# Performance work log

Hardware: AMD Instinct MI355X
Metric: run time of the kernel (lower is better)

The kernel has to match this reference:

```python
import jax, jax.numpy as jnp
import numpy as np

SIZE = 416
STRIDES = (8, 16, 32)
A = 3            # anchors per scale
C = 20           # num classes
CONF_THRESH = 0.001
NMS_THRESH = 0.5
ANCHORS = [[1.0,1.5],[2.0,3.0],[3.0,2.5],[1.5,3.5],[3.0,4.0],[4.0,3.0],[3.5,5.0],[5.0,4.5],[8.0,8.0]]


def _make_grids():
    # Mirrors myYOLOv3.init_grid, including the off-by-one that leaves the
    # LAST cell of each scale with zero anchor_wh (slice start:index).
    anchors = np.asarray(ANCHORS, np.float32).reshape(3, 3, 2)
    anchors = anchors * np.array([4.0, 2.0, 1.0], np.float32).reshape(3, 1, 1)
    grids, awhs, strs = [], [], []
    for i, s in enumerate(STRIDES):
        ws, hs = SIZE // s, SIZE // s
        ys, xs = np.meshgrid(np.arange(hs), np.arange(ws), indexing='ij')
        g = np.stack([xs, ys], -1).reshape(hs * ws, 1, 2).astype(np.float32)
        grids.append(np.broadcast_to(g, (hs * ws, A, 2)))
        awh = np.broadcast_to(anchors[i], (hs * ws, A, 2)).copy()
        awh[hs * ws - 1] = 0.0  # replicate init_grid bug
        awhs.append(awh)
        strs.append(np.full((hs * ws, A), s, np.float32))
    grid = jnp.asarray(np.concatenate(grids, 0))      # [HWt, A, 2]
    awh = jnp.asarray(np.concatenate(awhs, 0))        # [HWt, A, 2]
    stride = jnp.asarray(np.concatenate(strs, 0).reshape(-1))  # [HWt*A]
    return grid, awh, stride


def _flatten(pred):
    # [B, A*(1+C+4), H, W] -> obj [B, HW*A], cls [B, HW*A, C], xywh [B, HW, A, 4]
    B, abC, H, W = pred.shape
    p = jnp.transpose(pred, (0, 2, 3, 1)).reshape(B, H * W, abC)
    obj = p[..., :A].reshape(B, H * W * A)
    cls = p[..., A:A * (1 + C)].reshape(B, H * W * A, C)
    xywh = p[..., A * (1 + C):].reshape(B, H * W, A, 4)
    return obj, cls, xywh


def _nms(boxes, scores, cls_inds, valid):
    # Greedy per-class NMS: processing in global score order and suppressing
    # only same-class overlaps is exactly equivalent to the per-class loops
    # in myYOLOv3.postprocess.
    N = boxes.shape[0]
    order = jnp.argsort(-scores)
    b = boxes[order]
    c = cls_inds[order]
    v = valid[order]
    areas = (b[:, 2] - b[:, 0]) * (b[:, 3] - b[:, 1])
    idx = jnp.arange(N)

    def body(i, carry):
        keep, supp = carry
        ki = v[i] & ~supp[i]
        xx1 = jnp.maximum(b[i, 0], b[:, 0])
        yy1 = jnp.maximum(b[i, 1], b[:, 1])
        xx2 = jnp.minimum(b[i, 2], b[:, 2])
        yy2 = jnp.minimum(b[i, 3], b[:, 3])
        inter = jnp.maximum(1e-28, xx2 - xx1) * jnp.maximum(1e-28, yy2 - yy1)
        iou = inter / (areas[i] + areas - inter)
        supp = supp | (ki & (iou > NMS_THRESH) & (c == c[i]) & (idx > i))
        return keep.at[i].set(ki), supp

    keep_s, _ = jax.lax.fori_loop(
        0, N, body, (jnp.zeros(N, bool), jnp.zeros(N, bool)))
    return jnp.zeros(N, bool).at[order].set(keep_s)


def setup_inputs() -> dict:
    key = jax.random.key(0)
    k1, k2, k3 = jax.random.split(key, 3)
    B, abC = 64, A * (1 + 4 + C)
    return {
        'pred_1': jax.random.normal(k1, (B, abC, 52, 52), jnp.float32),
        'pred_2': jax.random.normal(k2, (B, abC, 26, 26), jnp.float32),
        'pred_3': jax.random.normal(k3, (B, abC, 13, 13), jnp.float32),
    }


def reference(pred_1, pred_2, pred_3):
    grid, awh, stride = _make_grids()
    objs, clss, xys = zip(*[_flatten(p) for p in (pred_1, pred_2, pred_3)])
    obj = jnp.concatenate(objs, 1)    # [B, N]
    cls = jnp.concatenate(clss, 1)    # [B, N, C]
    xywh = jnp.concatenate(xys, 1)    # [B, HWt, A, 4]
    B = obj.shape[0]

    # decode_boxes: sigmoid/exp + grid add + stride scale -> xyxy pixels
    cxy = jax.nn.sigmoid(xywh[..., :2]) + grid
    bwh = jnp.exp(xywh[..., 2:]) * awh
    bbox = jnp.concatenate([cxy, bwh], -1).reshape(B, -1, 4)  # [B, N, 4]
    half = bbox[..., 2:] * 0.5
    st = stride[None, :, None]
    boxes = jnp.concatenate([(bbox[..., :2] - half) * st,
                             (bbox[..., :2] + half) * st], -1)  # [B,N,4]

    all_obj = jax.nn.sigmoid(obj[0])                 # [N]
    all_bbox = boxes[0] / SIZE                       # normalized
    all_class = jax.nn.softmax(cls[0], axis=1) * all_obj[:, None]
    cls_inds = jnp.argmax(all_class, axis=1)
    scores = jnp.max(all_class, axis=1)
    valid = scores >= CONF_THRESH

    keep = _nms(all_bbox, scores, cls_inds, valid)

    # bboxes *= scale; clip to [0, SIZE-1]; /= scale
    bboxes = jnp.clip(all_bbox * SIZE, 0.0, SIZE - 1.0) / SIZE
    return bboxes, scores, cls_inds, keep
```

## Files before the change

kernel.cpp:

```cpp
#include <hip/hip_runtime.h>
#include <stdint.h>

typedef unsigned long long u64;
typedef unsigned int u32;

#define NA 10647
#define NCLS 20
#define CAPB 1024
#define CAP2 640
#define NWP 11
#define OUT_SCORES 42588
#define OUT_CLS    53235
#define OUT_KEEP   63882

__constant__ float c_aw[9] = {4.f,8.f,12.f, 3.f,6.f,8.f, 3.5f,5.f,8.f};
__constant__ float c_ah[9] = {6.f,12.f,10.f, 7.f,8.f,6.f, 5.f,4.5f,8.f};

__device__ __forceinline__ float sig(float x){ return 1.0f/(1.0f+expf(-x)); }

__device__ __forceinline__ u64 shflxor64(u64 v, int m){
    int lo = __shfl_xor((int)(u32)(v & 0xffffffffull), m);
    int hi = __shfl_xor((int)(u32)(v >> 32), m);
    return ((u64)(u32)hi << 32) | (u32)lo;
}

__global__ void decode_kernel(const float* __restrict__ p1, const float* __restrict__ p2,
                              const float* __restrict__ p3, float* __restrict__ out,
                              float4* __restrict__ box4, u64* __restrict__ bucket,
                              int* __restrict__ cls_cnt, float* __restrict__ keep_out)
{
    int n = blockIdx.x*128 + threadIdx.x;
    if (n >= NA) return;
    const float* p; int base, W, HW, L; float s;
    if (n < 8112)      { p=p1; base=0;     W=52; HW=2704; s=8.f;  L=0; }
    else if (n<10140)  { p=p2; base=8112;  W=26; HW=676;  s=16.f; L=1; }
    else               { p=p3; base=10140; W=13; HW=169;  s=32.f; L=2; }
    int r  = n - base;
    int hw = r/3, a = r - hw*3;
    int h  = hw/W, w = hw - h*W;

    float obj = sig(p[(size_t)a*HW + hw]);

    float e[NCLS];
    #pragma unroll
    for (int c=0;c<NCLS;c++) e[c] = p[(size_t)(3 + a*NCLS + c)*HW + hw];
    float xmax = e[0];
    #pragma unroll
    for (int c=1;c<NCLS;c++) xmax = fmaxf(xmax, e[c]);
    float ssum = 0.f;
    #pragma unroll
    for (int c=0;c<NCLS;c++){ e[c] = expf(e[c]-xmax); ssum += e[c]; }
    float best = -1.0f; int bi = 0;
    #pragma unroll
    for (int c=0;c<NCLS;c++){ float v = (e[c]/ssum)*obj; if (v > best){ best=v; bi=c; } }

    int xb = 63 + a*4;
    float tx = p[(size_t)(xb+0)*HW + hw];
    float ty = p[(size_t)(xb+1)*HW + hw];
    float tw = p[(size_t)(xb+2)*HW + hw];
    float th = p[(size_t)(xb+3)*HW + hw];
    float aw = c_aw[L*3+a], ah = c_ah[L*3+a];
    if (hw == HW-1){ aw=0.f; ah=0.f; }
    float cx = sig(tx) + (float)w;
    float cy = sig(ty) + (float)h;
    float bw = expf(tw)*aw, bh = expf(th)*ah;
    float hx = bw*0.5f,  hy = bh*0.5f;
    float x1 = ((cx-hx)*s)/416.0f;
    float y1 = ((cy-hy)*s)/416.0f;
    float x2 = ((cx+hx)*s)/416.0f;
    float y2 = ((cy+hy)*s)/416.0f;

    out[n*4+0] = fminf(fmaxf(x1*416.0f,0.f),415.f)/416.0f;
    out[n*4+1] = fminf(fmaxf(y1*416.0f,0.f),415.f)/416.0f;
    out[n*4+2] = fminf(fmaxf(x2*416.0f,0.f),415.f)/416.0f;
    out[n*4+3] = fminf(fmaxf(y2*416.0f,0.f),415.f)/416.0f;
    out[OUT_SCORES + n] = best;
    out[OUT_CLS    + n] = (float)bi;

    box4[n] = make_float4(x1,y1,x2,y2);

    u64 key = ((u64)(~__float_as_uint(best)) << 32) | (u32)n;
    int pos = atomicAdd(&cls_cnt[bi], 1);
    if (pos < CAPB) bucket[(size_t)bi*CAPB + pos] = key;
    else keep_out[n] = 0.0f;
}

__global__ __launch_bounds__(1024) void sort_kernel(
    const u64* __restrict__ bucket, const int* __restrict__ cls_cnt,
    const float4* __restrict__ box4, u64* __restrict__ skeys_g,
    float4* __restrict__ sbox_g)
{
    __shared__ u64 ex[CAPB];
    int b = blockIdx.x, t = threadIdx.x;
    int cnt = cls_cnt[b];
    int Mall = (cnt < CAPB) ? cnt : CAPB;
    u64 v = (t < Mall) ? bucket[(size_t)b*CAPB + t] : ~0ull;

    #pragma unroll
    for (int k = 2; k <= CAPB; k <<= 1){
        bool asc = ((t & k) == 0);
        for (int j = k >> 1; j >= 64; j >>= 1){
            ex[t] = v;
            __syncthreads();
            u64 w = ex[t ^ j];
            bool takeMin = (((t & j) == 0) == asc);
            v = takeMin ? (v < w ? v : w) : (v > w ? v : w);
            __syncthreads();
        }
        int j0 = (k >> 1 > 32) ? 32 : (k >> 1);
        #pragma unroll
        for (int j = j0; j >= 1; j >>= 1){
            u64 w = shflxor64(v, j);
            bool takeMin = (((t & j) == 0) == asc);
            v = takeMin ? (v < w ? v : w) : (v > w ? v : w);
        }
    }

    skeys_g[(size_t)b*CAPB + t] = v;
    if (t < CAP2){
        int M = (cnt < CAP2) ? cnt : CAP2;
        float4 bx = make_float4(0.f,0.f,0.f,0.f);
        if (t < M) bx = box4[(u32)v];
        sbox_g[(size_t)b*CAP2 + t] = bx;
    }
}

__global__ __launch_bounds__(256) void build_kernel(
    const float4* __restrict__ sbox_g, const int* __restrict__ cls_cnt,
    u64* __restrict__ maskg)
{
    __shared__ float4 cb_s[CAP2];
    __shared__ float  ca_s[CAP2];
    int rc = blockIdx.x, b = blockIdx.y;
    int tid = threadIdx.x, wv = tid>>6, ln = tid&63;
    int cnt = cls_cnt[b];
    int M  = (cnt < CAP2) ? cnt : CAP2;
    int MC = (M + 63) & ~63;
    if (rc*64 >= MC) return;
    for (int t = tid; t < CAP2; t += 256){
        float4 bx = sbox_g[(size_t)b*CAP2 + t];
        cb_s[t] = bx;
        ca_s[t] = (bx.z - bx.x) * (bx.w - bx.y);
    }
    __syncthreads();
    int nw = MC >> 6;
    for (int ri = wv; ri < 64; ri += 4){
        int rrow = rc*64 + ri;
        float4 rb = cb_s[rrow]; float ra = ca_s[rrow];
        for (int w = 0; w < nw; w++){
            int j = w*64 + ln;
            float4 cb = cb_s[j]; float ca = ca_s[j];
            float xx1=fmaxf(rb.x,cb.x), yy1=fmaxf(rb.y,cb.y);
            float xx2=fminf(rb.z,cb.z), yy2=fminf(rb.w,cb.w);
            float inter=fmaxf(1e-28f,xx2-xx1)*fmaxf(1e-28f,yy2-yy1);
            float iou = inter/((ra+ca)-inter);
            u64 bm = __ballot(iou > 0.5f);
            if (ln == 0) maskg[((size_t)b*CAP2 + rrow)*NWP + w] = bm;
        }
    }
}

__global__ __launch_bounds__(512) void scan_kernel(
    const u64* __restrict__ maskg, const u64* __restrict__ skeys_g,
    const int* __restrict__ cls_cnt, float* __restrict__ keep_out)
{
    __shared__ u64 lm[CAP2*NWP];
    __shared__ u64 validw_s[CAP2/64], remw[CAP2/64], keepw_s[CAP2/64];
    __shared__ u64 keep_bc;
    int b = blockIdx.x, tid = threadIdx.x, wv = tid>>6, ln = tid&63;
    int cnt = cls_cnt[b];
    int Mall = (cnt < CAPB) ? cnt : CAPB;
    int M    = (cnt < CAP2) ? cnt : CAP2;
    int MC = (M + 63) & ~63;
    int nw = MC >> 6;

    for (int t = tid; t < MC*NWP; t += 512) lm[t] = maskg[(size_t)b*CAP2*NWP + t];
    for (int w0 = wv; w0 < nw; w0 += 8){
        int t = w0*64 + ln;
        u64 key = skeys_g[(size_t)b*CAPB + t];
        float sc = __uint_as_float(~(u32)(key >> 32));
        u64 bm = __ballot(t < M && sc >= 0.001f);
        if (ln == 0) validw_s[w0] = bm;
    }
    for (int w = tid; w < nw; w += 512) remw[w] = 0ull;
    __syncthreads();

    for (int c = 0; c < nw; c++){
        if (wv == 0){
            u64 W = lm[(c*64 + ln)*NWP + c];
            u64 rem  = remw[c];
            u64 cand = validw_s[c] & ~rem;
            u64 keepw = 0;
            while (cand){
                int bp  = __builtin_ctzll(cand);
                int bps = __builtin_amdgcn_readfirstlane(bp);
                u64 rowm = ((u64)(u32)__builtin_amdgcn_readlane((int)(u32)(W>>32), bps) << 32)
                         |        (u32)__builtin_amdgcn_readlane((int)(u32)(W),     bps);
                keepw |= 1ull << bps;
                cand  &= ~(rowm | (1ull << bps));
            }
            if (ln == 0){ keepw_s[c] = keepw; keep_bc = keepw; }
        }
        __syncthreads();
        u64 kk = keep_bc;
        if (kk && c + 1 < nw){
            int i0 = tid >> 4;
            int wsl = tid & 15;
            int w = c + 1 + wsl;
            u64 acc = 0;
            if (w < nw){
                if ((kk >> i0) & 1ull)        acc  = lm[(c*64 + i0)*NWP + w];
                int i1 = i0 + 32;
                if ((kk >> i1) & 1ull)        acc |= lm[(c*64 + i1)*NWP + w];
            }
            acc |= shflxor64(acc, 16);
            acc |= shflxor64(acc, 32);
            if (ln < 16 && w < nw && acc) atomicOr(&remw[w], acc);
        }
        __syncthreads();
    }

    for (int t = tid; t < Mall; t += 512){
        u32 o = (u32)skeys_g[(size_t)b*CAPB + t];
        float kv = 0.0f;
        if (t < M) kv = ((keepw_s[t>>6] >> (t&63)) & 1ull) ? 1.0f : 0.0f;
        keep_out[o] = kv;
    }
}

extern "C" void kernel_launch(void* const* d_in, const int* in_sizes, int n_in,
                              void* d_out, int out_size, void* d_ws, size_t ws_size,
                              hipStream_t stream) {
    const float* p1 = (const float*)d_in[0];
    const float* p2 = (const float*)d_in[1];
    const float* p3 = (const float*)d_in[2];
    float* out = (float*)d_out;

    char* ws = (char*)d_ws;
    size_t off = 0;
    auto alloc = [&](size_t bytes)->void*{ void* p = ws + off; off += (bytes + 255) & ~(size_t)255; return p; };
    float4* box4    = (float4*)alloc((size_t)NA*16);
    u64*    bucket  = (u64*)   alloc((size_t)NCLS*CAPB*8);
    int*    cls_cnt = (int*)   alloc((size_t)NCLS*4);
    u64*    skeys_g = (u64*)   alloc((size_t)NCLS*CAPB*8);
    float4* sbox_g  = (float4*)alloc((size_t)NCLS*CAP2*16);
    u64*    maskg   = (u64*)   alloc((size_t)NCLS*CAP2*NWP*8);

    hipMemsetAsync(cls_cnt, 0, NCLS*sizeof(int), stream);
    decode_kernel<<<(NA+127)/128, 128, 0, stream>>>(p1,p2,p3,out,box4,bucket,cls_cnt,
                                                    out + OUT_KEEP);
    sort_kernel <<<NCLS, 1024, 0, stream>>>(bucket, cls_cnt, box4, skeys_g, sbox_g);
    build_kernel<<<dim3(CAP2/64, NCLS), 256, 0, stream>>>(sbox_g, cls_cnt, maskg);
    scan_kernel <<<NCLS, 512, 0, stream>>>(maskg, skeys_g, cls_cnt, out + OUT_KEEP);
}
```

Before: 181.7 us.

## Fuse sort, IoU mask build and NMS scan into one per-class kernel

Merges the sort, mask-build and scan kernels into one 1024-thread block per class. Sorted keys, boxes and the IoU mask now stay in shared memory instead of going through global memory, which removes two launches and their global round trips. The mask build also computes only the upper-triangle word range, skipping words before the row's own chunk. In exchange, the mask build now runs on 20 blocks instead of up to 200, which reduces parallelism, and the large shared-memory footprint limits occupancy.

```diff
diff --git a/kernel.cpp b/kernel.cpp
--- a/kernel.cpp
+++ b/kernel.cpp
@@ -85,17 +85,26 @@
     else keep_out[n] = 0.0f;
 }
 
-__global__ __launch_bounds__(1024) void sort_kernel(
+__global__ __launch_bounds__(1024) void nms_fused(
     const u64* __restrict__ bucket, const int* __restrict__ cls_cnt,
-    const float4* __restrict__ box4, u64* __restrict__ skeys_g,
-    float4* __restrict__ sbox_g)
+    const float4* __restrict__ box4, float* __restrict__ keep_out)
 {
-    __shared__ u64 ex[CAPB];
+    __shared__ u64    ex[CAPB];
+    __shared__ float4 cb_s[CAP2];
+    __shared__ float  ca_s[CAP2];
+    __shared__ u64    lm[CAP2*NWP];
+    __shared__ u64 validw_s[CAP2/64], remw[CAP2/64], keepw_s[CAP2/64];
+    __shared__ u64 keep_bc;
+
     int b = blockIdx.x, t = threadIdx.x;
+    int wv = t>>6, ln = t&63;
     int cnt = cls_cnt[b];
     int Mall = (cnt < CAPB) ? cnt : CAPB;
+    int M    = (cnt < CAP2) ? cnt : CAP2;
+    int MC = (M + 63) & ~63;
+    int nw = MC >> 6;
+
     u64 v = (t < Mall) ? bucket[(size_t)b*CAPB + t] : ~0ull;
-
     #pragma unroll
     for (int k = 2; k <= CAPB; k <<= 1){
         bool asc = ((t & k) == 0);
@@ -116,38 +125,24 @@
         }
     }
 
-    skeys_g[(size_t)b*CAPB + t] = v;
     if (t < CAP2){
-        int M = (cnt < CAP2) ? cnt : CAP2;
         float4 bx = make_float4(0.f,0.f,0.f,0.f);
         if (t < M) bx = box4[(u32)v];
-        sbox_g[(size_t)b*CAP2 + t] = bx;
-    }
-}
-
-__global__ __launch_bounds__(256) void build_kernel(
-    const float4* __restrict__ sbox_g, const int* __restrict__ cls_cnt,
-    u64* __restrict__ maskg)
-{
-    __shared__ float4 cb_s[CAP2];
-    __shared__ float  ca_s[CAP2];
-    int rc = blockIdx.x, b = blockIdx.y;
-    int tid = threadIdx.x, wv = tid>>6, ln = tid&63;
-    int cnt = cls_cnt[b];
-    int M  = (cnt < CAP2) ? cnt : CAP2;
-    int MC = (M + 63) & ~63;
-    if (rc*64 >= MC) return;
-    for (int t = tid; t < CAP2; t += 256){
-        float4 bx = sbox_g[(size_t)b*CAP2 + t];
         cb_s[t] = bx;
         ca_s[t] = (bx.z - bx.x) * (bx.w - bx.y);
     }
+    if (t < MC){
+        float sc = __uint_as_float(~(u32)(v >> 32));
+        u64 bm = __ballot(t < M && sc >= 0.001f);
+        if (ln == 0) validw_s[t>>6] = bm;
+    }
+    if (t < CAP2/64) remw[t] = 0ull;
     __syncthreads();
-    int nw = MC >> 6;
-    for (int ri = wv; ri < 64; ri += 4){
-        int rrow = rc*64 + ri;
-        float4 rb = cb_s[rrow]; float ra = ca_s[rrow];
-        for (int w = 0; w < nw; w++){
+
+    for (int r = wv; r < MC; r += 16){
+        int rc = r >> 6;
+        float4 rb = cb_s[r]; float ra = ca_s[r];
+        for (int w = rc; w < nw; w++){
             int j = w*64 + ln;
             float4 cb = cb_s[j]; float ca = ca_s[j];
             float xx1=fmaxf(rb.x,cb.x), yy1=fmaxf(rb.y,cb.y);
@@ -155,34 +150,9 @@
             float inter=fmaxf(1e-28f,xx2-xx1)*fmaxf(1e-28f,yy2-yy1);
             float iou = inter/((ra+ca)-inter);
             u64 bm = __ballot(iou > 0.5f);
-            if (ln == 0) maskg[((size_t)b*CAP2 + rrow)*NWP + w] = bm;
-        }
-    }
-}
-
-__global__ __launch_bounds__(512) void scan_kernel(
-    const u64* __restrict__ maskg, const u64* __restrict__ skeys_g,
-    const int* __restrict__ cls_cnt, float* __restrict__ keep_out)
-{
-    __shared__ u64 lm[CAP2*NWP];
-    __shared__ u64 validw_s[CAP2/64], remw[CAP2/64], keepw_s[CAP2/64];
-    __shared__ u64 keep_bc;
-    int b = blockIdx.x, tid = threadIdx.x, wv = tid>>6, ln = tid&63;
-    int cnt = cls_cnt[b];
-    int Mall = (cnt < CAPB) ? cnt : CAPB;
-    int M    = (cnt < CAP2) ? cnt : CAP2;
-    int MC = (M + 63) & ~63;
-    int nw = MC >> 6;
-
-    for (int t = tid; t < MC*NWP; t += 512) lm[t] = maskg[(size_t)b*CAP2*NWP + t];
-    for (int w0 = wv; w0 < nw; w0 += 8){
-        int t = w0*64 + ln;
-        u64 key = skeys_g[(size_t)b*CAPB + t];
-        float sc = __uint_as_float(~(u32)(key >> 32));
-        u64 bm = __ballot(t < M && sc >= 0.001f);
-        if (ln == 0) validw_s[w0] = bm;
-    }
-    for (int w = tid; w < nw; w += 512) remw[w] = 0ull;
+            if (ln == 0) lm[r*NWP + w] = bm;
+        }
+    }
     __syncthreads();
 
     for (int c = 0; c < nw; c++){
@@ -204,15 +174,11 @@
         __syncthreads();
         u64 kk = keep_bc;
         if (kk && c + 1 < nw){
-            int i0 = tid >> 4;
-            int wsl = tid & 15;
+            int i   = t >> 4;
+            int wsl = t & 15;
             int w = c + 1 + wsl;
             u64 acc = 0;
-            if (w < nw){
-                if ((kk >> i0) & 1ull)        acc  = lm[(c*64 + i0)*NWP + w];
-                int i1 = i0 + 32;
-                if ((kk >> i1) & 1ull)        acc |= lm[(c*64 + i1)*NWP + w];
-            }
+            if (w < nw && ((kk >> i) & 1ull)) acc = lm[(c*64 + i)*NWP + w];
             acc |= shflxor64(acc, 16);
             acc |= shflxor64(acc, 32);
             if (ln < 16 && w < nw && acc) atomicOr(&remw[w], acc);
@@ -220,11 +186,10 @@
         __syncthreads();
     }
 
-    for (int t = tid; t < Mall; t += 512){
-        u32 o = (u32)skeys_g[(size_t)b*CAPB + t];
+    if (t < Mall){
         float kv = 0.0f;
         if (t < M) kv = ((keepw_s[t>>6] >> (t&63)) & 1ull) ? 1.0f : 0.0f;
-        keep_out[o] = kv;
+        keep_out[(u32)v] = kv;
     }
 }
 
@@ -242,14 +207,9 @@
     float4* box4    = (float4*)alloc((size_t)NA*16);
     u64*    bucket  = (u64*)   alloc((size_t)NCLS*CAPB*8);
     int*    cls_cnt = (int*)   alloc((size_t)NCLS*4);
-    u64*    skeys_g = (u64*)   alloc((size_t)NCLS*CAPB*8);
-    float4* sbox_g  = (float4*)alloc((size_t)NCLS*CAP2*16);
-    u64*    maskg   = (u64*)   alloc((size_t)NCLS*CAP2*NWP*8);
 
     hipMemsetAsync(cls_cnt, 0, NCLS*sizeof(int), stream);
     decode_kernel<<<(NA+127)/128, 128, 0, stream>>>(p1,p2,p3,out,box4,bucket,cls_cnt,
                                                     out + OUT_KEEP);
-    sort_kernel <<<NCLS, 1024, 0, stream>>>(bucket, cls_cnt, box4, skeys_g, sbox_g);
-    build_kernel<<<dim3(CAP2/64, NCLS), 256, 0, stream>>>(sbox_g, cls_cnt, maskg);
-    scan_kernel <<<NCLS, 512, 0, stream>>>(maskg, skeys_g, cls_cnt, out + OUT_KEEP);
-}
+    nms_fused   <<<NCLS, 1024, 0, stream>>>(bucket, cls_cnt, box4, out + OUT_KEEP);
+}
```

After: 200.6 us. 1.1x slower.
